# Kernel optimization log

Hardware: AMD Instinct MI355X
Metric: run time of the kernel (lower is better)

## Reference

```python
import jax, jax.numpy as jnp
import numpy as np

DIM_IN = 768
HEADS = 12
DIM_HEAD = 64
SCALE = DIM_HEAD ** (-0.5)


def setup_inputs() -> dict:
    key = jax.random.key(0)
    k_x, k_qkv, k_out = jax.random.split(key, 3)
    B, N = 2, 2048
    x = jax.random.normal(k_x, (B, N, DIM_IN), dtype=jnp.float32)
    # w_qkv: Linear(dim_in, 3*heads*dim_head, bias=False); stored as [in, out] for x @ W
    w_qkv = jax.random.normal(k_qkv, (DIM_IN, HEADS * 3 * DIM_HEAD), dtype=jnp.float32) * (DIM_IN ** -0.5)
    # merge_heads Linear(heads*dim_head, dim_in) with bias
    w_out = jax.random.normal(k_out, (HEADS * DIM_HEAD, DIM_IN), dtype=jnp.float32) * ((HEADS * DIM_HEAD) ** -0.5)
    b_out = jnp.zeros((DIM_IN,), dtype=jnp.float32)
    return {"x": x, "w_qkv": w_qkv, "w_out": w_out, "b_out": b_out}


def reference(x, w_qkv, w_out, b_out):
    B, N, _ = x.shape
    qkv = x @ w_qkv                                   # [B, N, H*3*Dh]
    qkv = qkv.reshape(B, N, HEADS, 3, DIM_HEAD)       # matches torch reshape order
    q = jnp.transpose(qkv[:, :, :, 0, :], (0, 2, 1, 3))  # [B, H, N, Dh]
    k = jnp.transpose(qkv[:, :, :, 1, :], (0, 2, 1, 3))
    v = jnp.transpose(qkv[:, :, :, 2, :], (0, 2, 1, 3))
    scores = jnp.einsum("bhnd,bhmd->bhnm", q, k) * SCALE  # full N x N score matrix
    attn = jax.nn.softmax(scores, axis=-1)
    ctx = jnp.einsum("bhnm,bhmd->bhnd", attn, v)          # [B, H, N, Dh]
    heads = jnp.transpose(ctx, (0, 2, 1, 3)).reshape(B, N, HEADS * DIM_HEAD)
    out = heads @ w_out + b_out                            # dropout is identity at inference
    return out
```

## Files before the change

### kernel.cpp

```cpp
#include <hip/hip_runtime.h>

#define SEQ   2048
#define BATCH 2
#define DIN   768
#define NH    12
#define DH    64
#define QKVN  (NH*3*DH)
#define NBH   (BATCH*NH)
#define QSCALE 0.18033688011112042f

typedef __attribute__((ext_vector_type(8))) short short8;
typedef __attribute__((ext_vector_type(4))) float float4v;

__device__ __forceinline__ ushort f2bf(float f) {
  union { float f; uint u; } v; v.f = f;
  return (ushort)((v.u + 0x7fffu + ((v.u >> 16) & 1u)) >> 16);
}

__device__ __forceinline__ void gld_lds16(const void* g, void* l) {
  __builtin_amdgcn_global_load_lds(
      (__attribute__((address_space(1))) unsigned int*)(g),
      (__attribute__((address_space(3))) unsigned int*)(l), 16, 0, 0);
}

__global__ __launch_bounds__(256) void cvt_x(const float* __restrict__ X,
                                             ushort* __restrict__ Xb) {
  int i = blockIdx.x * 256 + threadIdx.x;
  float4 v = ((const float4*)X)[i];
  ushort4 o;
  o.x = f2bf(v.x); o.y = f2bf(v.y); o.z = f2bf(v.z); o.w = f2bf(v.w);
  ((ushort4*)Xb)[i] = o;
}

__global__ __launch_bounds__(256) void cvt_T(const float* __restrict__ W,
                                             ushort* __restrict__ WT,
                                             int Kdim, int Ndim) {
  __shared__ float tile[32][33];
  const int tx = threadIdx.x & 31, tg = threadIdx.x >> 5;
  const int r0 = blockIdx.x * 32, c0 = blockIdx.y * 32;
#pragma unroll
  for (int i = 0; i < 4; ++i) {
    int r = tg + i * 8;
    tile[r][tx] = W[(size_t)(r0 + r) * Ndim + c0 + tx];
  }
  __syncthreads();
#pragma unroll
  for (int i = 0; i < 4; ++i) {
    int c = tg + i * 8;
    WT[(size_t)(c0 + c) * Kdim + r0 + tx] = f2bf(tile[tx][c]);
  }
}

#define GEMM_CORE(Abf, BT)                                                     \
  __shared__ ushort As[8192];                                                  \
  __shared__ ushort Bs[8192];                                                  \
  const int t = threadIdx.x;                                                   \
  const int lane = t & 63, wid = t >> 6;                                       \
  const int wr = wid >> 1, wc = wid & 1;                                       \
  const int m0 = blockIdx.x * 128, n0 = blockIdx.y * 128;                      \
  float4v acc[4][4] = {};                                                      \
  for (int k0 = 0; k0 < DIN; k0 += 64) {                                       \
    __syncthreads();                                                           \
    _Pragma("unroll")                                                          \
    for (int i = 0; i < 4; ++i) {                                              \
      int s   = t + i * 256;                                                   \
      int sub = s >> 7, kss = (s >> 6) & 1, l = s & 63;                        \
      int row = sub * 16 + (l & 15);                                           \
      int kc  = kss * 32 + (l >> 4) * 8;                                       \
      int lb  = (i * 256 + wid * 64) * 8;           \
      gld_lds16(&Abf[(size_t)(m0 + row) * DIN + k0 + kc], &As[lb]);            \
      gld_lds16(&BT[(size_t)(n0 + row) * DIN + k0 + kc], &Bs[lb]);             \
    }                                                                          \
    __syncthreads();                                                           \
    _Pragma("unroll")                                                          \
    for (int ks = 0; ks < 2; ++ks) {                                           \
      short8 a[4], b[4];                                                       \
      _Pragma("unroll")                                                        \
      for (int mi = 0; mi < 4; ++mi)                                           \
        a[mi] = *(const short8*)&As[(((wr * 4 + mi) * 2 + ks) * 64 + lane) * 8];\
      _Pragma("unroll")                                                        \
      for (int ni = 0; ni < 4; ++ni)                                           \
        b[ni] = *(const short8*)&Bs[(((wc * 4 + ni) * 2 + ks) * 64 + lane) * 8];\
      _Pragma("unroll")                                                        \
      for (int mi = 0; mi < 4; ++mi)                                           \
        _Pragma("unroll")                                                      \
        for (int ni = 0; ni < 4; ++ni)                                         \
          acc[mi][ni] = __builtin_amdgcn_mfma_f32_16x16x32_bf16(               \
              a[mi], b[ni], acc[mi][ni], 0, 0, 0);                             \
    }                                                                          \
  }

__global__ __launch_bounds__(256) void gemm_qkv(const ushort* __restrict__ Abf,
                                                const ushort* __restrict__ BT,
                                                ushort* __restrict__ Q,
                                                ushort* __restrict__ K,
                                                ushort* __restrict__ Vt) {
  GEMM_CORE(Abf, BT)
  const int mbase = m0 + wr * 64;
#pragma unroll
  for (int ni = 0; ni < 4; ++ni) {
    const int cbase = n0 + wc * 64 + ni * 16;
    const int h = cbase / 192, rem = cbase % 192;
    const int which = rem / 64;
    const int d0 = (rem % 64) + (lane & 15);
#pragma unroll
    for (int mi = 0; mi < 4; ++mi) {
      const int mrow = mbase + mi * 16 + (lane >> 4) * 4;
      const int bb = mrow >> 11, n = mrow & (SEQ - 1);
      const int bh = bb * NH + h;
      if (which == 2) {
        ushort4 pk;
        pk.x = f2bf(acc[mi][ni][0]); pk.y = f2bf(acc[mi][ni][1]);
        pk.z = f2bf(acc[mi][ni][2]); pk.w = f2bf(acc[mi][ni][3]);
        *(ushort4*)&Vt[((size_t)bh * DH + d0) * SEQ + n] = pk;
      } else {
        ushort* dst = (which == 0) ? Q : K;
        const float sc = (which == 0) ? QSCALE : 1.0f;
#pragma unroll
        for (int r = 0; r < 4; ++r)
          dst[((size_t)bh * SEQ + n + r) * DH + d0] = f2bf(acc[mi][ni][r] * sc);
      }
    }
  }
}

__global__ __launch_bounds__(256) void gemm_out(const ushort* __restrict__ Abf,
                                                const ushort* __restrict__ BT,
                                                const float* __restrict__ bias,
                                                float* __restrict__ Out) {
  GEMM_CORE(Abf, BT)
#pragma unroll
  for (int ni = 0; ni < 4; ++ni) {
    const int c = n0 + wc * 64 + ni * 16 + (lane & 15);
    const float bv = bias[c];
#pragma unroll
    for (int mi = 0; mi < 4; ++mi) {
      const int mrow = m0 + wr * 64 + mi * 16 + (lane >> 4) * 4;
#pragma unroll
      for (int r = 0; r < 4; ++r)
        Out[(size_t)(mrow + r) * DIN + c] = acc[mi][ni][r] + bv;
    }
  }
}

__global__ __launch_bounds__(256) void attn(const ushort* __restrict__ Q,
                                            const ushort* __restrict__ K,
                                            const ushort* __restrict__ Vt,
                                            ushort* __restrict__ CTX) {
  __shared__ ushort Ks[2][4096];
  __shared__ ushort Vs[2][4096];
  __shared__ ushort ps[4][1024];
  const int t = threadIdx.x, lane = t & 63, wid = t >> 6;
  const int lo = lane & 15, hi = lane >> 4;
  const int bid = blockIdx.x;
  const int bh = bid % NBH;
  const int q0 = (bid / NBH) * 64 + wid * 16;
  const size_t base = (size_t)bh * SEQ * DH;
  const ushort* Kg = K + base;
  const ushort* Vg = Vt + (size_t)bh * DH * SEQ;
  ushort* myps = ps[wid];

  short8 qf[2];
#pragma unroll
  for (int ks = 0; ks < 2; ++ks)
    qf[ks] = *(const short8*)&Q[base + (size_t)(q0 + lo) * DH + ks * 32 + hi * 8];

  float4v Ot[4] = {};
  float mrun = -1e30f, lrun = 0.f;

#pragma unroll
  for (int i = 0; i < 2; ++i) {
    int c = t + i * 256;
    int g = c ^ ((c >> 3) & 7);
    int lb = (i * 256 + wid * 64) * 8;
    gld_lds16(&Kg[g * 8], &Ks[0][lb]);
    gld_lds16(&Vg[(size_t)(g >> 3) * SEQ + (g & 7) * 8], &Vs[0][lb]);
  }
  __syncthreads();

  const int NT = SEQ / 64;
  for (int kt = 0; kt < NT; ++kt) {
    const int cur = kt & 1;
    const char* Kl = (const char*)&Ks[cur][0];
    const char* Vl = (const char*)&Vs[cur][0];
    if (kt + 1 < NT) {
      const int key0n = (kt + 1) * 64;
#pragma unroll
      for (int i = 0; i < 2; ++i) {
        int c = t + i * 256;
        int g = c ^ ((c >> 3) & 7);
        int lb = (i * 256 + wid * 64) * 8;
        gld_lds16(&Kg[(size_t)key0n * DH + g * 8], &Ks[cur ^ 1][lb]);
        gld_lds16(&Vg[(size_t)(g >> 3) * SEQ + key0n + (g & 7) * 8],
                  &Vs[cur ^ 1][lb]);
      }
    }
    float4v st[4];
#pragma unroll
    for (int ns = 0; ns < 4; ++ns) {
      st[ns] = (float4v){0.f, 0.f, 0.f, 0.f};
#pragma unroll
      for (int ks = 0; ks < 2; ++ks) {
        int row = ns * 16 + lo;
        int byte = (row * 128 + ks * 64 + hi * 16) ^ ((row & 7) << 4);
        short8 kf = *(const short8*)(Kl + byte);
        st[ns] = __builtin_amdgcn_mfma_f32_16x16x32_bf16(kf, qf[ks], st[ns], 0, 0, 0);
      }
    }
    float mx = fmaxf(fmaxf(fmaxf(st[0][0], st[0][1]), fmaxf(st[0][2], st[0][3])),
                     fmaxf(fmaxf(st[1][0], st[1][1]), fmaxf(st[1][2], st[1][3])));
    mx = fmaxf(mx, fmaxf(fmaxf(fmaxf(st[2][0], st[2][1]), fmaxf(st[2][2], st[2][3])),
                         fmaxf(fmaxf(st[3][0], st[3][1]), fmaxf(st[3][2], st[3][3]))));
    mx = fmaxf(mx, __shfl_xor(mx, 16));
    mx = fmaxf(mx, __shfl_xor(mx, 32));
    if (!__all(mx <= mrun + 8.0f)) {
      float mnew  = fmaxf(mrun, mx);
      float alpha = exp2f(mrun - mnew);
      lrun *= alpha;
#pragma unroll
      for (int ns = 0; ns < 4; ++ns)
#pragma unroll
        for (int r = 0; r < 4; ++r) Ot[ns][r] *= alpha;
      mrun = mnew;
    }
    float p[4][4];
    float rs = 0.f;
#pragma unroll
    for (int ns = 0; ns < 4; ++ns)
#pragma unroll
      for (int r = 0; r < 4; ++r) {
        p[ns][r] = exp2f(st[ns][r] - mrun);
        rs += p[ns][r];
      }
    rs += __shfl_xor(rs, 16);
    rs += __shfl_xor(rs, 32);
    lrun += rs;
#pragma unroll
    for (int ns = 0; ns < 4; ++ns) {
      uint2 d2;
      d2.x = __builtin_amdgcn_perm(__float_as_uint(p[ns][1]),
                                   __float_as_uint(p[ns][0]), 0x07060302u);
      d2.y = __builtin_amdgcn_perm(__float_as_uint(p[ns][3]),
                                   __float_as_uint(p[ns][2]), 0x07060302u);
      int byte = (lo * 128 + ns * 32 + hi * 8) ^ ((lo & 7) << 4);
      *(uint2*)((char*)myps + byte) = d2;
    }
    asm volatile("s_waitcnt lgkmcnt(0)" ::: "memory");
    short8 pf[2];
#pragma unroll
    for (int ks = 0; ks < 2; ++ks) {
      int byte = (lo * 128 + ks * 64 + hi * 16) ^ ((lo & 7) << 4);
      pf[ks] = *(const short8*)((char*)myps + byte);
    }
    __builtin_amdgcn_s_setprio(1);
#pragma unroll
    for (int ns = 0; ns < 4; ++ns)
#pragma unroll
      for (int ks = 0; ks < 2; ++ks) {
        int row = ns * 16 + lo;
        int byte = (row * 128 + ks * 64 + hi * 16) ^ ((row & 7) << 4);
        short8 vf = *(const short8*)(Vl + byte);
        Ot[ns] = __builtin_amdgcn_mfma_f32_16x16x32_bf16(vf, pf[ks], Ot[ns], 0, 0, 0);
      }
    __builtin_amdgcn_s_setprio(0);
    __syncthreads();
  }
  const int bb = bh / NH, h = bh % NH;
  const float inv = 1.0f / lrun;
  const int n = q0 + lo;
#pragma unroll
  for (int ns = 0; ns < 4; ++ns) {
    ushort4 o;
    o.x = f2bf(Ot[ns][0] * inv); o.y = f2bf(Ot[ns][1] * inv);
    o.z = f2bf(Ot[ns][2] * inv); o.w = f2bf(Ot[ns][3] * inv);
    *(ushort4*)&CTX[(size_t)(bb * SEQ + n) * DIN + h * DH + ns * 16 + hi * 4] = o;
  }
}

extern "C" void kernel_launch(void* const* d_in, const int* in_sizes, int n_in,
                              void* d_out, int out_size, void* d_ws, size_t ws_size,
                              hipStream_t stream) {
  const float* x     = (const float*)d_in[0];
  const float* w_qkv = (const float*)d_in[1];
  const float* w_out = (const float*)d_in[2];
  const float* b_out = (const float*)d_in[3];
  float* out = (float*)d_out;

  ushort* ws = (ushort*)d_ws;
  const size_t nX   = (size_t)BATCH * SEQ * DIN;
  const size_t nWq  = (size_t)DIN * QKVN;
  const size_t nWo  = (size_t)DIN * DIN;
  const size_t nQKV = (size_t)BATCH * NH * SEQ * DH;

  ushort* xb   = ws;
  ushort* wqT  = xb + nX;
  ushort* woT  = wqT + nWq;
  ushort* Qb   = woT + nWo;
  ushort* Kb   = Qb + nQKV;
  ushort* Vt   = Kb + nQKV;
  ushort* CTX  = Vt + nQKV;

  cvt_x<<<dim3(nX / 4 / 256), 256, 0, stream>>>(x, xb);
  cvt_T<<<dim3(DIN / 32, QKVN / 32), 256, 0, stream>>>(w_qkv, wqT, DIN, QKVN);
  cvt_T<<<dim3(DIN / 32, DIN / 32), 256, 0, stream>>>(w_out, woT, DIN, DIN);

  gemm_qkv<<<dim3(BATCH * SEQ / 128, QKVN / 128), 256, 0, stream>>>(
      xb, wqT, Qb, Kb, Vt);
  attn<<<dim3(SEQ / 64 * NBH), 256, 0, stream>>>(Qb, Kb, Vt, CTX);
  gemm_out<<<dim3(BATCH * SEQ / 128, DIN / 128), 256, 0, stream>>>(
      CTX, woT, b_out, out);
}
```

Measured before the change: 210.5 us.

## Merge conversion kernels, stage Q/K epilogue through LDS, hoist attention offsets

Folds the three fp32-to-bf16 conversion launches into one kernel that picks its role from the block index, removing two launches. The QKV GEMM epilogue now writes Q and K tiles into shared-memory scratch and stores contiguous 32-byte rows, replacing scattered 2-byte global stores. The attention kernel precomputes swizzled LDS offsets and the K/V prefetch pointers outside the loop to cut per-iteration integer math. These add shared-memory traffic and extra waits in the epilogue, and keep more registers live in the attention loop.

New measurement: 208.9 us. No clear change (-0.7%).

```diff
diff --git a/kernel.cpp b/kernel.cpp
--- a/kernel.cpp
+++ b/kernel.cpp
@@ -23,21 +23,28 @@
       (__attribute__((address_space(3))) unsigned int*)(l), 16, 0, 0);
 }
 
-__global__ __launch_bounds__(256) void cvt_x(const float* __restrict__ X,
-                                             ushort* __restrict__ Xb) {
-  int i = blockIdx.x * 256 + threadIdx.x;
-  float4 v = ((const float4*)X)[i];
-  ushort4 o;
-  o.x = f2bf(v.x); o.y = f2bf(v.y); o.z = f2bf(v.z); o.w = f2bf(v.w);
-  ((ushort4*)Xb)[i] = o;
-}
-
-__global__ __launch_bounds__(256) void cvt_T(const float* __restrict__ W,
-                                             ushort* __restrict__ WT,
-                                             int Kdim, int Ndim) {
+__global__ __launch_bounds__(256) void cvt_all(const float* __restrict__ X,
+                                               ushort* __restrict__ Xb,
+                                               const float* __restrict__ Wq,
+                                               ushort* __restrict__ WqT,
+                                               const float* __restrict__ Wo,
+                                               ushort* __restrict__ WoT) {
   __shared__ float tile[32][33];
+  const int bid = blockIdx.x;
+  if (bid < 3072) {
+    int i = bid * 256 + threadIdx.x;
+    float4 v = ((const float4*)X)[i];
+    ushort4 o;
+    o.x = f2bf(v.x); o.y = f2bf(v.y); o.z = f2bf(v.z); o.w = f2bf(v.w);
+    ((ushort4*)Xb)[i] = o;
+    return;
+  }
+  const float* W; ushort* WT; int Ndim, idx;
+  if (bid < 3072 + 1728) { idx = bid - 3072; W = Wq; WT = WqT; Ndim = QKVN; }
+  else                   { idx = bid - 4800; W = Wo; WT = WoT; Ndim = DIN;  }
+  const int bx = idx % (DIN / 32), by = idx / (DIN / 32);
+  const int r0 = bx * 32, c0 = by * 32;
   const int tx = threadIdx.x & 31, tg = threadIdx.x >> 5;
-  const int r0 = blockIdx.x * 32, c0 = blockIdx.y * 32;
 #pragma unroll
   for (int i = 0; i < 4; ++i) {
     int r = tg + i * 8;
@@ -47,7 +54,7 @@
 #pragma unroll
   for (int i = 0; i < 4; ++i) {
     int c = tg + i * 8;
-    WT[(size_t)(c0 + c) * Kdim + r0 + tx] = f2bf(tile[tx][c]);
+    WT[(size_t)(c0 + c) * DIN + r0 + tx] = f2bf(tile[tx][c]);
   }
 }
 
@@ -96,30 +103,52 @@
                                                 ushort* __restrict__ K,
                                                 ushort* __restrict__ Vt) {
   GEMM_CORE(Abf, BT)
+  __syncthreads();
+  ushort* scr = &As[wid * 1024];
+  const int eL = lane & 15, eH = lane >> 4;
+  const int cb64  = n0 + wc * 64;
+  const int h     = cb64 / 192;
+  const int which = (cb64 % 192) / 64;
   const int mbase = m0 + wr * 64;
-#pragma unroll
-  for (int ni = 0; ni < 4; ++ni) {
-    const int cbase = n0 + wc * 64 + ni * 16;
-    const int h = cbase / 192, rem = cbase % 192;
-    const int which = rem / 64;
-    const int d0 = (rem % 64) + (lane & 15);
-#pragma unroll
-    for (int mi = 0; mi < 4; ++mi) {
-      const int mrow = mbase + mi * 16 + (lane >> 4) * 4;
-      const int bb = mrow >> 11, n = mrow & (SEQ - 1);
-      const int bh = bb * NH + h;
-      if (which == 2) {
+  if (which == 2) {
+#pragma unroll
+    for (int ni = 0; ni < 4; ++ni) {
+      const int d0 = ni * 16 + eL;
+#pragma unroll
+      for (int mi = 0; mi < 4; ++mi) {
+        const int mrow = mbase + mi * 16 + eH * 4;
+        const int bb = mrow >> 11, n = mrow & (SEQ - 1);
+        const int bhv = bb * NH + h;
         ushort4 pk;
         pk.x = f2bf(acc[mi][ni][0]); pk.y = f2bf(acc[mi][ni][1]);
         pk.z = f2bf(acc[mi][ni][2]); pk.w = f2bf(acc[mi][ni][3]);
-        *(ushort4*)&Vt[((size_t)bh * DH + d0) * SEQ + n] = pk;
-      } else {
-        ushort* dst = (which == 0) ? Q : K;
-        const float sc = (which == 0) ? QSCALE : 1.0f;
+        *(ushort4*)&Vt[((size_t)bhv * DH + d0) * SEQ + n] = pk;
+      }
+    }
+  } else {
+    ushort* dst = (which == 0) ? Q : K;
+    const float sc = (which == 0) ? QSCALE : 1.0f;
+    const int rr = lane >> 2;
+    const int rb = (lane & 3) ^ (rr >> 2);
+    const int roff = rr * 64 + rb * 16;
+#pragma unroll
+    for (int mi = 0; mi < 4; ++mi) {
+      const int mrow = mbase + mi * 16;
+      const int bb = mrow >> 11, nb = mrow & (SEQ - 1);
+#pragma unroll
+      for (int ni = 0; ni < 4; ++ni) {
+        const int sb = ((ni ^ eH) & 3) * 16;
 #pragma unroll
         for (int r = 0; r < 4; ++r)
-          dst[((size_t)bh * SEQ + n + r) * DH + d0] = f2bf(acc[mi][ni][r] * sc);
-      }
+          scr[(eH * 4 + r) * 64 + sb + eL] = f2bf(acc[mi][ni][r] * sc);
+      }
+      asm volatile("s_waitcnt lgkmcnt(0)" ::: "memory");
+      short8 v0 = *(const short8*)&scr[roff];
+      short8 v1 = *(const short8*)&scr[roff + 8];
+      ushort* gp = dst + ((size_t)(bb * NH + h) * SEQ + nb) * DH + lane * 16;
+      *(short8*)&gp[0] = v0;
+      *(short8*)&gp[8] = v1;
+      asm volatile("s_waitcnt lgkmcnt(0)" ::: "memory");
     }
   }
 }
@@ -156,9 +185,31 @@
   const int bh = bid % NBH;
   const int q0 = (bid / NBH) * 64 + wid * 16;
   const size_t base = (size_t)bh * SEQ * DH;
-  const ushort* Kg = K + base;
-  const ushort* Vg = Vt + (size_t)bh * DH * SEQ;
   ushort* myps = ps[wid];
+
+  int kvoff[4][2];
+#pragma unroll
+  for (int ns = 0; ns < 4; ++ns)
+#pragma unroll
+    for (int ks = 0; ks < 2; ++ks) {
+      int row = ns * 16 + lo;
+      kvoff[ns][ks] = (row * 128 + ks * 64 + hi * 16) ^ ((row & 7) << 4);
+    }
+  int pwoff[4], proff[2];
+#pragma unroll
+  for (int ns = 0; ns < 4; ++ns)
+    pwoff[ns] = (lo * 128 + ns * 32 + hi * 8) ^ ((lo & 7) << 4);
+#pragma unroll
+  for (int ks = 0; ks < 2; ++ks)
+    proff[ks] = (lo * 128 + ks * 64 + hi * 16) ^ ((lo & 7) << 4);
+
+  const int c0i = t, c1i = t + 256;
+  const int g0 = c0i ^ ((c0i >> 3) & 7), g1 = c1i ^ ((c1i >> 3) & 7);
+  const int lb0 = (wid * 64) * 8, lb1 = (256 + wid * 64) * 8;
+  const ushort* kp0 = K + base + g0 * 8;
+  const ushort* kp1 = K + base + g1 * 8;
+  const ushort* vp0 = Vt + (size_t)bh * DH * SEQ + (size_t)(g0 >> 3) * SEQ + (g0 & 7) * 8;
+  const ushort* vp1 = Vt + (size_t)bh * DH * SEQ + (size_t)(g1 >> 3) * SEQ + (g1 & 7) * 8;
 
   short8 qf[2];
 #pragma unroll
@@ -168,32 +219,24 @@
   float4v Ot[4] = {};
   float mrun = -1e30f, lrun = 0.f;
 
-#pragma unroll
-  for (int i = 0; i < 2; ++i) {
-    int c = t + i * 256;
-    int g = c ^ ((c >> 3) & 7);
-    int lb = (i * 256 + wid * 64) * 8;
-    gld_lds16(&Kg[g * 8], &Ks[0][lb]);
-    gld_lds16(&Vg[(size_t)(g >> 3) * SEQ + (g & 7) * 8], &Vs[0][lb]);
-  }
+  gld_lds16(kp0, &Ks[0][lb0]);
+  gld_lds16(kp1, &Ks[0][lb1]);
+  gld_lds16(vp0, &Vs[0][lb0]);
+  gld_lds16(vp1, &Vs[0][lb1]);
+  kp0 += 64 * DH; kp1 += 64 * DH; vp0 += 64; vp1 += 64;
   __syncthreads();
 
   const int NT = SEQ / 64;
   for (int kt = 0; kt < NT; ++kt) {
-    const int cur = kt & 1;
+    const int cur = kt & 1, nb = cur ^ 1;
     const char* Kl = (const char*)&Ks[cur][0];
     const char* Vl = (const char*)&Vs[cur][0];
     if (kt + 1 < NT) {
-      const int key0n = (kt + 1) * 64;
-#pragma unroll
-      for (int i = 0; i < 2; ++i) {
-        int c = t + i * 256;
-        int g = c ^ ((c >> 3) & 7);
-        int lb = (i * 256 + wid * 64) * 8;
-        gld_lds16(&Kg[(size_t)key0n * DH + g * 8], &Ks[cur ^ 1][lb]);
-        gld_lds16(&Vg[(size_t)(g >> 3) * SEQ + key0n + (g & 7) * 8],
-                  &Vs[cur ^ 1][lb]);
-      }
+      gld_lds16(kp0, &Ks[nb][lb0]);
+      gld_lds16(kp1, &Ks[nb][lb1]);
+      gld_lds16(vp0, &Vs[nb][lb0]);
+      gld_lds16(vp1, &Vs[nb][lb1]);
+      kp0 += 64 * DH; kp1 += 64 * DH; vp0 += 64; vp1 += 64;
     }
     float4v st[4];
 #pragma unroll
@@ -201,9 +244,7 @@
       st[ns] = (float4v){0.f, 0.f, 0.f, 0.f};
 #pragma unroll
       for (int ks = 0; ks < 2; ++ks) {
-        int row = ns * 16 + lo;
-        int byte = (row * 128 + ks * 64 + hi * 16) ^ ((row & 7) << 4);
-        short8 kf = *(const short8*)(Kl + byte);
+        short8 kf = *(const short8*)(Kl + kvoff[ns][ks]);
         st[ns] = __builtin_amdgcn_mfma_f32_16x16x32_bf16(kf, qf[ks], st[ns], 0, 0, 0);
       }
     }
@@ -242,24 +283,19 @@
                                    __float_as_uint(p[ns][0]), 0x07060302u);
       d2.y = __builtin_amdgcn_perm(__float_as_uint(p[ns][3]),
                                    __float_as_uint(p[ns][2]), 0x07060302u);
-      int byte = (lo * 128 + ns * 32 + hi * 8) ^ ((lo & 7) << 4);
-      *(uint2*)((char*)myps + byte) = d2;
+      *(uint2*)((char*)myps + pwoff[ns]) = d2;
     }
     asm volatile("s_waitcnt lgkmcnt(0)" ::: "memory");
     short8 pf[2];
 #pragma unroll
-    for (int ks = 0; ks < 2; ++ks) {
-      int byte = (lo * 128 + ks * 64 + hi * 16) ^ ((lo & 7) << 4);
-      pf[ks] = *(const short8*)((char*)myps + byte);
-    }
+    for (int ks = 0; ks < 2; ++ks)
+      pf[ks] = *(const short8*)((char*)myps + proff[ks]);
     __builtin_amdgcn_s_setprio(1);
 #pragma unroll
     for (int ns = 0; ns < 4; ++ns)
 #pragma unroll
       for (int ks = 0; ks < 2; ++ks) {
-        int row = ns * 16 + lo;
-        int byte = (row * 128 + ks * 64 + hi * 16) ^ ((row & 7) << 4);
-        short8 vf = *(const short8*)(Vl + byte);
+        short8 vf = *(const short8*)(Vl + kvoff[ns][ks]);
         Ot[ns] = __builtin_amdgcn_mfma_f32_16x16x32_bf16(vf, pf[ks], Ot[ns], 0, 0, 0);
       }
     __builtin_amdgcn_s_setprio(0);
@@ -300,10 +336,7 @@
   ushort* Vt   = Kb + nQKV;
   ushort* CTX  = Vt + nQKV;
 
-  cvt_x<<<dim3(nX / 4 / 256), 256, 0, stream>>>(x, xb);
-  cvt_T<<<dim3(DIN / 32, QKVN / 32), 256, 0, stream>>>(w_qkv, wqT, DIN, QKVN);
-  cvt_T<<<dim3(DIN / 32, DIN / 32), 256, 0, stream>>>(w_out, woT, DIN, DIN);
-
+  cvt_all<<<dim3(5376), 256, 0, stream>>>(x, xb, w_qkv, wqT, w_out, woT);
   gemm_qkv<<<dim3(BATCH * SEQ / 128, QKVN / 128), 256, 0, stream>>>(
       xb, wqT, Qb, Kb, Vt);
   attn<<<dim3(SEQ / 64 * NBH), 256, 0, stream>>>(Qb, Kb, Vt, CTX);
```
